# Performance work log

Measured on AMD Instinct MI355X. Metric: run time of the kernel, lower is better.

The kernel has to match this reference:

```python
import jax, jax.numpy as jnp
import numpy as np

ALPHA = 0.2  # LeakyReLU negative slope
NEG_INF = -1e30


def _gat_layer(h, adj_mask, W, a, concat):
    # h: [N, Fin], W: [Fin, Fout], a: [2*Fout]
    Wh = h @ W                      # [N, Fout]
    F = W.shape[1]
    # e_ij = LeakyReLU(a[:F] . Wh_i + a[F:] . Wh_j)  -- equivalent to the
    # concat([Wh_i, Wh_j]) @ a formulation, without the N*N*2F tensor.
    src = Wh @ a[:F]                # [N]
    dst = Wh @ a[F:]                # [N]
    e = src[:, None] + dst[None, :]  # [N, N]
    e = jnp.where(e > 0, e, ALPHA * e)  # LeakyReLU
    e = jnp.where(adj_mask, e, NEG_INF)
    att = jax.nn.softmax(e, axis=1)  # [N, N]; dropout inactive (eval mode)
    h_prime = att @ Wh               # [N, Fout]
    return jax.nn.elu(h_prime) if concat else h_prime


def setup_inputs() -> dict:
    key = jax.random.key(0)
    ks = jax.random.split(key, 6)
    N, nfeat, nhid, nheads, nout = 4096, 512, 256, 4, 256
    x = jax.random.normal(ks[0], (N, nfeat), dtype=jnp.float32)
    adj = jax.random.randint(ks[1], (N, N), 0, 2, dtype=jnp.int32)
    W1 = jax.random.normal(ks[2], (nheads, nfeat, nhid), dtype=jnp.float32) * 0.05
    a1 = jax.random.normal(ks[3], (nheads, 2 * nhid), dtype=jnp.float32) * 0.05
    W2 = jax.random.normal(ks[4], (nhid * nheads, nout), dtype=jnp.float32) * 0.05
    a2 = jax.random.normal(ks[5], (2 * nout,), dtype=jnp.float32) * 0.05
    return {"x": x, "adj": adj, "W1": W1, "a1": a1, "W2": W2, "a2": a2}


def reference(x, adj, W1, a1, W2, a2):
    adj_mask = adj != 0  # [N, N] bool
    # Multi-head first layer (concat=True, ELU), vmapped over heads.
    heads = jax.vmap(lambda W, a: _gat_layer(x, adj_mask, W, a, True))(W1, a1)
    # heads: [nheads, N, nhid] -> concat along features: [N, nheads*nhid]
    h = jnp.transpose(heads, (1, 0, 2)).reshape(x.shape[0], -1)
    # Output attention layer (concat=False).
    return _gat_layer(h, adj_mask, W2, a2, False)
```

## Files before the change

kernel.cpp:

```cpp
#include <hip/hip_runtime.h>
#include <hip/hip_bf16.h>
#include <stdint.h>

#define ALPHA 0.2f
#define LOG2E 1.4426950408889634f

typedef __attribute__((ext_vector_type(4))) float f32x4;
typedef __attribute__((ext_vector_type(8))) __bf16 bf16x8;
typedef __attribute__((ext_vector_type(8))) unsigned short u16x8;
typedef __attribute__((ext_vector_type(4))) unsigned short u16x4;
typedef __attribute__((ext_vector_type(4))) unsigned int u32x4;

static __device__ __forceinline__ unsigned short f2bf(float f) {
  unsigned u = __builtin_bit_cast(unsigned, f);
  u += 0x7FFFu + ((u >> 16) & 1u);
  return (unsigned short)(u >> 16);
}
static __device__ __forceinline__ float bf2f(unsigned short h) {
  unsigned u = ((unsigned)h) << 16;
  return __builtin_bit_cast(float, u);
}
static __device__ __forceinline__ float exp2_hw(float x) {
  float r; asm("v_exp_f32 %0, %1" : "=v"(r) : "v"(x)); return r;
}
static __device__ __forceinline__ unsigned int cvt_pk_bf16(float lo, float hi) {
  unsigned int r; asm("v_cvt_pk_bf16_f32 %0, %1, %2" : "=v"(r) : "v"(lo), "v"(hi)); return r;
}
static __device__ __forceinline__ void gl_lds16(const void* g, void* lds) {
  __builtin_amdgcn_global_load_lds(
      (const __attribute__((address_space(1))) unsigned int*)g,
      (__attribute__((address_space(3))) unsigned int*)lds, 16, 0, 0);
}

#define PREP_PACK_END 65536
#define PREP_CAST_END 66560
#define PREP_T1_END   67072
#define PREP_T2_END   67328
#define PREP_WA1_END  67840
#define PREP_GRID     68096

__global__ void k_prep_all(const int* __restrict__ adj, unsigned int* __restrict__ bits,
                           const float* __restrict__ x, unsigned short* __restrict__ xb,
                           const float* __restrict__ W1, unsigned short* __restrict__ w1t,
                           const float* __restrict__ W2, unsigned short* __restrict__ w2t,
                           const float* __restrict__ a1, float* __restrict__ wa1,
                           const float* __restrict__ a2, float* __restrict__ wa2) {
  __shared__ float tsh[32][33];
  const int b = blockIdx.x, tid = threadIdx.x;
  if (b < PREP_PACK_END) {
    int gid  = b * 4 + (tid >> 6);
    int lane = tid & 63;
    int i   = gid >> 6;
    int w64 = gid & 63;
    int j = (w64 << 6) | lane;
    int v = adj[(long)i * 4096 + j];
    unsigned long long m = __ballot(v != 0);
    if (lane == 0) {
      bits[i * 128 + 2 * w64]     = (unsigned int)m;
      bits[i * 128 + 2 * w64 + 1] = (unsigned int)(m >> 32);
    }
  } else if (b < PREP_CAST_END) {
    int t = (b - PREP_PACK_END) * 256 + tid;
    const f32x4* p = (const f32x4*)(x + (long)t * 8);
    f32x4 va = p[0], vb = p[1];
    u16x8 o;
#pragma unroll
    for (int k = 0; k < 4; ++k) { o[k] = f2bf(va[k]); o[k + 4] = f2bf(vb[k]); }
    *(u16x8*)(xb + (long)t * 8) = o;
  } else if (b < PREP_T2_END) {
    const float* in; unsigned short* out; int K, N, bx, by, bz;
    if (b < PREP_T1_END) {
      int idx = b - PREP_CAST_END;
      bx = idx & 15; by = (idx >> 4) & 7; bz = idx >> 7;
      in = W1; out = w1t; K = 512; N = 256;
    } else {
      int idx = b - PREP_T1_END;
      bx = idx & 31; by = (idx >> 5) & 7; bz = 0;
      in = W2; out = w2t; K = 1024; N = 256;
    }
    long bs = (long)K * N;
    const float* inb = in + bz * bs;
    unsigned short* outb = out + bz * bs;
    int k0 = bx * 32, n0 = by * 32;
    int tx = tid & 31, ty = tid >> 5;
#pragma unroll
    for (int it = 0; it < 4; ++it)
      tsh[ty + it * 8][tx] = inb[(long)(k0 + ty + it * 8) * N + n0 + tx];
    __syncthreads();
#pragma unroll
    for (int it = 0; it < 4; ++it)
      outb[(long)(n0 + ty + it * 8) * K + k0 + tx] = f2bf(tsh[tx][ty + it * 8]);
  } else {
    const float* W; const float* a; float* wa; int headK;
    int bl;
    if (b < PREP_WA1_END) { bl = b - PREP_T2_END; W = W1; a = a1; wa = wa1; headK = 512; }
    else                  { bl = b - PREP_WA1_END; W = W2; a = a2; wa = wa2; headK = 1024; }
    const int F = 256;
    int w = (bl * 256 + tid) >> 6;
    int lane = tid & 63;
    int h = w / headK, fl = w % headK;
    const float* row = W + (size_t)w * F;
    const float* ah = a + (size_t)h * 2 * F;
    float s0 = 0.f, s1 = 0.f;
    for (int fo = lane; fo < F; fo += 64) {
      float wv = row[fo];
      s0 += wv * ah[fo];
      s1 += wv * ah[F + fo];
    }
#pragma unroll
    for (int off = 32; off; off >>= 1) {
      s0 += __shfl_xor(s0, off);
      s1 += __shfl_xor(s1, off);
    }
    if (lane == 0) {
      wa[(size_t)(h * 2 + 0) * headK + fl] = s0;
      wa[(size_t)(h * 2 + 1) * headK + fl] = s1;
    }
  }
}

static __device__ __forceinline__ void gemm_wh_body(
    const unsigned short* __restrict__ A, const unsigned short* __restrict__ BT,
    unsigned short* __restrict__ whT, int K, int i0, int fbase,
    unsigned short* As, unsigned short* Bs) {
  const int tid = threadIdx.x, lane = tid & 63, wid = tid >> 6;
  const int q = lane >> 4, l15 = lane & 15;
  const int wm = wid >> 1, wn = wid & 1;
  f32x4 acc[2][4] = {};
  const unsigned short* aRow = A + (long)(i0 + (tid >> 2)) * K + (tid & 3) * 8;
  for (int kk = 0; kk < K; kk += 32) {
    __syncthreads();
    gl_lds16(aRow + kk, (char*)As + tid * 16);
#pragma unroll
    for (int half = 0; half < 2; ++half) {
      int cid = half * 256 + tid;
      gl_lds16(BT + (long)(fbase + (cid >> 2)) * K + kk + (cid & 3) * 8,
               (char*)Bs + cid * 16);
    }
    __syncthreads();
    bf16x8 af[2], bfr[4];
#pragma unroll
    for (int mi = 0; mi < 2; ++mi)
      af[mi] = *(const bf16x8*)&As[(wm * 32 + mi * 16 + l15) * 32 + q * 8];
#pragma unroll
    for (int ni = 0; ni < 4; ++ni)
      bfr[ni] = *(const bf16x8*)&Bs[(wn * 64 + ni * 16 + l15) * 32 + q * 8];
#pragma unroll
    for (int mi = 0; mi < 2; ++mi)
#pragma unroll
      for (int ni = 0; ni < 4; ++ni)
        acc[mi][ni] = __builtin_amdgcn_mfma_f32_16x16x32_bf16(af[mi], bfr[ni], acc[mi][ni], 0, 0, 0);
  }
#pragma unroll
  for (int mi = 0; mi < 2; ++mi)
#pragma unroll
    for (int ni = 0; ni < 4; ++ni) {
      int ig = i0 + wm * 32 + mi * 16 + q * 4;
      int fg = fbase + wn * 64 + ni * 16 + l15;
      u16x4 v;
#pragma unroll
      for (int r = 0; r < 4; ++r) v[r] = f2bf(acc[mi][ni][r]);
      *(u16x4*)&whT[(long)fg * 4096 + ig] = v;
    }
}

__global__ void __launch_bounds__(256, 4)
k_l1(const unsigned short* __restrict__ xb, const unsigned short* __restrict__ w1t,
     unsigned short* __restrict__ whT1, const float* __restrict__ wa,
     float* __restrict__ srcv, float* __restrict__ dstv, float* __restrict__ dstva) {
  __shared__ unsigned short As[64 * 32];
  __shared__ unsigned short Bs[128 * 32];
  const int b = blockIdx.x;
  if (b < 512) {
    int i0 = (b & 63) * 64;
    int fbase = (b >> 7) * 256 + ((b >> 6) & 1) * 128;
    gemm_wh_body(xb, w1t, whT1, 512, i0, fbase, As, Bs);
    return;
  }
  const int mb = b - 512;
  int lane = threadIdx.x & 63, wid = threadIdx.x >> 6;
  float wv[8][8];
#pragma unroll
  for (int v = 0; v < 8; ++v)
#pragma unroll
    for (int j = 0; j < 8; ++j) wv[v][j] = wa[v * 512 + lane * 8 + j];
  int base = (mb * 4 + wid) * 4;
  for (int rr = 0; rr < 4; ++rr) {
    int i = base + rr;
    u16x8 xv = *(const u16x8*)(xb + (size_t)i * 512 + lane * 8);
    float xf[8];
#pragma unroll
    for (int j = 0; j < 8; ++j) xf[j] = bf2f(xv[j]);
    float s[8] = {};
#pragma unroll
    for (int v = 0; v < 8; ++v)
#pragma unroll
      for (int j = 0; j < 8; ++j) s[v] += xf[j] * wv[v][j];
#pragma unroll
    for (int v = 0; v < 8; ++v)
#pragma unroll
      for (int off = 32; off; off >>= 1) s[v] += __shfl_xor(s[v], off);
    if (lane == 0) {
#pragma unroll
      for (int h = 0; h < 4; ++h) {
        srcv[h * 4096 + i] = s[h * 2] * LOG2E;
        float d = s[h * 2 + 1] * LOG2E;
        dstv[h * 4096 + i] = d;
        dstva[h * 4096 + i] = ALPHA * d;
      }
    }
  }
}

__global__ void __launch_bounds__(256, 4)
k_l2(const unsigned short* __restrict__ h1, const unsigned short* __restrict__ w2t,
     unsigned short* __restrict__ whT2, const float* __restrict__ wa,
     float* __restrict__ srcv, float* __restrict__ dstv, float* __restrict__ dstva) {
  __shared__ unsigned short As[64 * 32];
  __shared__ unsigned short Bs[128 * 32];
  const int b = blockIdx.x;
  if (b < 128) {
    int i0 = (b & 63) * 64;
    int fbase = ((b >> 6) & 1) * 128;
    gemm_wh_body(h1, w2t, whT2, 1024, i0, fbase, As, Bs);
    return;
  }
  const int mb = b - 128;
  int lane = threadIdx.x & 63, wid = threadIdx.x >> 6;
  float wv[2][16];
#pragma unroll
  for (int v = 0; v < 2; ++v)
#pragma unroll
    for (int j = 0; j < 16; ++j) wv[v][j] = wa[v * 1024 + lane * 16 + j];
  int base = (mb * 4 + wid) * 4;
  for (int rr = 0; rr < 4; ++rr) {
    int i = base + rr;
    u16x8 x0 = *(const u16x8*)(h1 + (size_t)i * 1024 + lane * 16);
    u16x8 x1 = *(const u16x8*)(h1 + (size_t)i * 1024 + lane * 16 + 8);
    float s0 = 0.f, s1 = 0.f;
#pragma unroll
    for (int j = 0; j < 8; ++j) {
      float a0 = bf2f(x0[j]), a1 = bf2f(x1[j]);
      s0 += a0 * wv[0][j] + a1 * wv[0][j + 8];
      s1 += a0 * wv[1][j] + a1 * wv[1][j + 8];
    }
#pragma unroll
    for (int off = 32; off; off >>= 1) {
      s0 += __shfl_xor(s0, off);
      s1 += __shfl_xor(s1, off);
    }
    if (lane == 0) {
      srcv[i] = s0 * LOG2E;
      float d = s1 * LOG2E;
      dstv[i] = d;
      dstva[i] = ALPHA * d;
    }
  }
}


#define STAGE(PAR)                                                             \
  _Pragma("unroll")                                                            \
  for (int it = 0; it < 8; ++it)                                               \
    gl_lds16(wh_head + sidx + it * 131072u,                                    \
             (char*)&Bs[PAR][0] + (it * 256 + tid) * 16);                      \
  sidx += 64;

#define PREFETCH(DZ, DA, WB)                                                   \
  _Pragma("unroll")                                                            \
  for (int c4 = 0; c4 < 4; ++c4) {                                             \
    DZ[c4] = *(const f32x4*)(dzp + c4 * 4);                                    \
    DA[c4] = *(const f32x4*)(dap + c4 * 4);                                    \
  }                                                                            \
  WB = *browp;                                                                 \
  dzp += 64; dap += 64; browp += 2;

#define PCOMP(WB, DZ, DA)                                                      \
  {                                                                            \
    unsigned wbv = (WB >> shift) & 0xFFFFu;                                    \
    _Pragma("unroll")                                                          \
    for (int c8 = 0; c8 < 2; ++c8) {                                           \
      float pe[8];                                                             \
      _Pragma("unroll")                                                        \
      for (int jj = 0; jj < 8; ++jj) {                                         \
        float e = fmaxf(sm + DZ[c8 * 2 + (jj >> 2)][jj & 3],                   \
                        am + DA[c8 * 2 + (jj >> 2)][jj & 3]);                  \
        e = (wbv & (1u << (c8 * 8 + jj))) ? e : -1e30f;                        \
        pe[jj] = exp2_hw(e);                                                   \
      }                                                                        \
      u32x4 pv;                                                                \
      pv[0] = cvt_pk_bf16(pe[0], pe[1]);                                       \
      pv[1] = cvt_pk_bf16(pe[2], pe[3]);                                       \
      pv[2] = cvt_pk_bf16(pe[4], pe[5]);                                       \
      pv[3] = cvt_pk_bf16(pe[6], pe[7]);                                       \
      lsum += ((pe[0] + pe[1]) + (pe[2] + pe[3])) +                            \
              ((pe[4] + pe[5]) + (pe[6] + pe[7]));                             \
      if (c8) pvB = pv; else pvA = pv;                                         \
    }                                                                          \
  }

#define PSTO(PAR)                                                              \
  *(u32x4*)&Ps[PAR][prow * 64 + ((2 * kq + 0) ^ (prow & 7)) * 8] = pvA;        \
  *(u32x4*)&Ps[PAR][prow * 64 + ((2 * kq + 1) ^ (prow & 7)) * 8] = pvB;

#define DOMFMA(PAR)                                                            \
  {                                                                            \
    _Pragma("unroll")                                                          \
    for (int s = 0; s < 2; ++s) {                                              \
      bf16x8 af[4], bfr[4];                                                    \
      _Pragma("unroll")                                                        \
      for (int mi = 0; mi < 4; ++mi)                                           \
        af[mi] = *(const bf16x8*)&Ps[PAR][(mi * 16 + l15) * 64 +               \
                                          ((s * 4 + q) ^ (l15 & 7)) * 8];      \
      _Pragma("unroll")                                                        \
      for (int ni = 0; ni < 4; ++ni) {                                         \
        int f = wid * 64 + ni * 16 + l15;                                      \
        int slot = (s * 4 + q) ^ (l15 & 7);                                    \
        bfr[ni] = *(const bf16x8*)&Bs[PAR][f * 64 + slot * 8];                 \
      }                                                                        \
      __builtin_amdgcn_s_setprio(1);                                           \
      _Pragma("unroll")                                                        \
      for (int mi = 0; mi < 4; ++mi)                                           \
        _Pragma("unroll")                                                      \
        for (int ni = 0; ni < 4; ++ni)                                         \
          acc[mi][ni] = __builtin_amdgcn_mfma_f32_16x16x32_bf16(               \
              af[mi], bfr[ni], acc[mi][ni], 0, 0, 0);                          \
      __builtin_amdgcn_s_setprio(0);                                           \
    }                                                                          \
  }

#define STEP_SYNC                                                              \
  asm volatile("s_waitcnt vmcnt(9)" ::: "memory");                             \
  asm volatile("s_waitcnt lgkmcnt(0)" ::: "memory");                           \
  __builtin_amdgcn_sched_barrier(0);                                           \
  __builtin_amdgcn_s_barrier();                                                \
  __builtin_amdgcn_sched_barrier(0);

#define BODY(PAR, DZC, DAC, WBC, DZN, DAN, WBN)                                \
  {                                                                            \
    STAGE(PAR ^ 1)                                                             \
    __builtin_amdgcn_sched_barrier(0);     \
    PREFETCH(DZN, DAN, WBN)                                                    \
    PCOMP(WBC, DZC, DAC)                                                       \
    DOMFMA(PAR)                                                                \
    PSTO(PAR ^ 1)                                                              \
    STEP_SYNC                                                                  \
  }

template <int JS, int H, int OC>
__global__ void __launch_bounds__(256, 2)
k_attn4(const unsigned short* __restrict__ whT, const unsigned int* __restrict__ bits,
        const float* __restrict__ srcv, const float* __restrict__ dstv,
        const float* __restrict__ dstva,
        float* __restrict__ Opart, float* __restrict__ Lpart) {
  static_assert(H * JS == 8, "group size must be 8");
  __shared__ unsigned short Bs[2][256 * 64];
  __shared__ unsigned short Ps[2][64 * 64];
  const int tid = threadIdx.x, lane = tid & 63, wid = tid >> 6;
  const int q = lane >> 4, l15 = lane & 15;
  const int bid = blockIdx.x;
  const int g = bid & 7;
  const int head = g & (H - 1);
  const int js = g / H;
  const int i0 = (bid >> 3) * 64;
  const int jbase = js * (4096 / JS);
  constexpr int JSTEPS = (4096 / JS) / 64;

  const unsigned short* wh_head = whT + (size_t)head * 256 * 4096;
  const int prow = tid & 63, kq = tid >> 6;

  float dmax;
  {
    float* dred = (float*)&Ps[0][0];
    const float* dp = dstv + head * 4096;
    float lm = -1e30f;
#pragma unroll
    for (int k = 0; k < 4; ++k) {
      f32x4 v = *(const f32x4*)(dp + (tid + k * 256) * 4);
      lm = fmaxf(fmaxf(lm, fmaxf(v[0], v[1])), fmaxf(v[2], v[3]));
    }
#pragma unroll
    for (int off = 32; off; off >>= 1) lm = fmaxf(lm, __shfl_xor(lm, off));
    if (lane == 0) dred[wid] = lm;
    __syncthreads();
    dmax = fmaxf(fmaxf(dred[0], dred[1]), fmaxf(dred[2], dred[3]));
    __syncthreads();
  }

  float src_r = srcv[head * 4096 + i0 + prow];
  float m_r;
  { float xm = src_r + dmax; m_r = fmaxf(xm, ALPHA * xm); }
  const float sm = src_r - m_r;
  const float am = ALPHA * src_r - m_r;
  float lsum = 0.f;
  f32x4 acc[4][4] = {};

  const int srow = tid >> 3;
  unsigned sidx = (unsigned)(srow * 4096 + jbase + ((tid & 7) ^ (srow & 7)) * 8);
  const float* dzp = dstv + head * 4096 + jbase + kq * 16;
  const float* dap = dstva + head * 4096 + jbase + kq * 16;
  const unsigned int* browp = bits + (size_t)(i0 + prow) * 128 + (jbase >> 5) + (kq >> 1);
  const int shift = (kq & 1) * 16;

  f32x4 dzA[4], daA[4], dzB[4], daB[4];
  unsigned wbA, wbB;
  u32x4 pvA, pvB;

  PREFETCH(dzA, daA, wbA)
  __builtin_amdgcn_sched_barrier(0);
  STAGE(0)
  __builtin_amdgcn_sched_barrier(0);
  PREFETCH(dzB, daB, wbB)
  PCOMP(wbA, dzA, daA)
  PSTO(0)
  STEP_SYNC

  for (int t = 0; t < JSTEPS - 3; t += 2) {
    BODY(0, dzB, daB, wbB, dzA, daA, wbA)
    BODY(1, dzA, daA, wbA, dzB, daB, wbB)
  }
  BODY(0, dzB, daB, wbB, dzA, daA, wbA)
  DOMFMA(1)

  __syncthreads();
  float* Lred = (float*)&Ps[0][0];
  Lred[kq * 64 + prow] = lsum;
  __syncthreads();
  if (tid < 64)
    Lpart[(size_t)(js * H + head) * 4096 + i0 + tid] =
        Lred[tid] + Lred[64 + tid] + Lred[128 + tid] + Lred[192 + tid];
  float* Ob = Opart + (size_t)js * 4096 * OC + head * 256;
#pragma unroll
  for (int mi = 0; mi < 4; ++mi)
#pragma unroll
    for (int ni = 0; ni < 4; ++ni) {
      int i = i0 + mi * 16 + q * 4;
      int col = wid * 64 + ni * 16 + l15;
#pragma unroll
      for (int r = 0; r < 4; ++r)
        Ob[(size_t)(i + r) * OC + col] = acc[mi][ni][r];
    }
}

__global__ void __launch_bounds__(256) k_comb1(const float* __restrict__ Op,
                                               const float* __restrict__ Lp,
                                               unsigned short* __restrict__ h1) {
  int gidx = blockIdx.x * 256 + threadIdx.x;
  int i = gidx >> 8, c0 = (gidx & 255) * 4;
  int h = c0 >> 8;
  float l = Lp[h * 4096 + i] + Lp[(4 + h) * 4096 + i];
  float inv = 1.f / l;
  f32x4 p0 = *(const f32x4*)(Op + (size_t)i * 1024 + c0);
  f32x4 p1 = *(const f32x4*)(Op + (size_t)4096 * 1024 + (size_t)i * 1024 + c0);
  u16x4 o;
#pragma unroll
  for (int r = 0; r < 4; ++r) {
    float v = (p0[r] + p1[r]) * inv;
    v = v > 0.f ? v : (__expf(v) - 1.f);
    o[r] = f2bf(v);
  }
  *(u16x4*)(h1 + (size_t)i * 1024 + c0) = o;
}

__global__ void __launch_bounds__(256) k_comb2(const float* __restrict__ Op,
                                               const float* __restrict__ Lp,
                                               float* __restrict__ out) {
  int gidx = blockIdx.x * 256 + threadIdx.x;
  int i = gidx >> 6, c0 = (gidx & 63) * 4;
  float l = 0.f;
#pragma unroll
  for (int js = 0; js < 8; ++js) l += Lp[js * 4096 + i];
  f32x4 s = {0.f, 0.f, 0.f, 0.f};
#pragma unroll
  for (int js = 0; js < 8; ++js)
    s += *(const f32x4*)(Op + (size_t)js * 4096 * 256 + (size_t)i * 256 + c0);
  float inv = 1.f / l;
  f32x4 o;
#pragma unroll
  for (int r = 0; r < 4; ++r) o[r] = s[r] * inv;
  *(f32x4*)(out + (size_t)i * 256 + c0) = o;
}

extern "C" void kernel_launch(void* const* d_in, const int* in_sizes, int n_in,
                              void* d_out, int out_size, void* d_ws, size_t ws_size,
                              hipStream_t stream) {
  const float* x  = (const float*)d_in[0];
  const int* adj  = (const int*)d_in[1];
  const float* W1 = (const float*)d_in[2];
  const float* a1 = (const float*)d_in[3];
  const float* W2 = (const float*)d_in[4];
  const float* a2 = (const float*)d_in[5];

  char* ws = (char*)d_ws;
  size_t off = 0;
  auto alloc = [&](size_t bytes) {
    void* p = ws + off;
    off = (off + bytes + 255) & ~(size_t)255;
    return p;
  };
  unsigned int*   bits = (unsigned int*)  alloc((size_t)4096 * 128 * 4);
  unsigned short* xb   = (unsigned short*)alloc((size_t)4096 * 512 * 2);
  unsigned short* w1t  = (unsigned short*)alloc((size_t)4 * 256 * 512 * 2);
  unsigned short* w2t  = (unsigned short*)alloc((size_t)256 * 1024 * 2);
  unsigned short* whT1 = (unsigned short*)alloc((size_t)1024 * 4096 * 2);
  unsigned short* h1   = (unsigned short*)alloc((size_t)4096 * 1024 * 2);
  unsigned short* whT2 = (unsigned short*)alloc((size_t)256 * 4096 * 2);
  float* wa1  = (float*)alloc((size_t)8 * 512 * 4);
  float* wa2  = (float*)alloc((size_t)2 * 1024 * 4);
  float* src1 = (float*)alloc(4 * 4096 * 4);
  float* dst1 = (float*)alloc(4 * 4096 * 4);
  float* dst1a = (float*)alloc(4 * 4096 * 4);
  float* src2 = (float*)alloc(4096 * 4);
  float* dst2 = (float*)alloc(4096 * 4);
  float* dst2a = (float*)alloc(4096 * 4);
  float* Lp1  = (float*)alloc((size_t)8 * 4096 * 4);
  float* Lp2  = (float*)alloc((size_t)8 * 4096 * 4);
  float* Opart = (float*)alloc((size_t)2 * 4096 * 1024 * 4);

  k_prep_all<<<dim3(PREP_GRID), dim3(256), 0, stream>>>(
      adj, bits, x, xb, W1, w1t, W2, w2t, a1, wa1, a2, wa2);

  k_l1<<<dim3(768), dim3(256), 0, stream>>>(xb, w1t, whT1, wa1, src1, dst1, dst1a);
  k_attn4<2, 4, 1024><<<dim3(512), dim3(256), 0, stream>>>(whT1, bits, src1, dst1, dst1a, Opart, Lp1);
  k_comb1<<<dim3(4096), dim3(256), 0, stream>>>(Opart, Lp1, h1);

  k_l2<<<dim3(384), dim3(256), 0, stream>>>(h1, w2t, whT2, wa2, src2, dst2, dst2a);
  k_attn4<8, 1, 256><<<dim3(512), dim3(256), 0, stream>>>(whT2, bits, src2, dst2, dst2a, Opart, Lp2);
  k_comb2<<<dim3(1024), dim3(256), 0, stream>>>(Opart, Lp2, (float*)d_out);
}
```

Before: 246.5 us.

## Double-buffer Wh GEMM LDS staging and move adjacency bit-packing into layer-1 kernel

The Wh GEMM body now double-buffers its global-to-LDS tiles. It prefetches the next K-slice while running MFMAs on the current one, and uses one barrier per iteration instead of two. The adjacency bit-packing moves out of the prep kernel into extra blocks of k_l1, where each block reads int4 vectors and packs nibbles through LDS instead of using per-wave ballots. The goal is to hide load latency in the GEMM and to overlap the bandwidth-heavy adj read with GEMM work. The cost is larger LDS use per block and a bigger k_l1 grid that mixes heterogeneous work.

```diff
diff --git a/kernel.cpp b/kernel.cpp
--- a/kernel.cpp
+++ b/kernel.cpp
@@ -32,35 +32,21 @@
       (__attribute__((address_space(3))) unsigned int*)lds, 16, 0, 0);
 }
 
-#define PREP_PACK_END 65536
-#define PREP_CAST_END 66560
-#define PREP_T1_END   67072
-#define PREP_T2_END   67328
-#define PREP_WA1_END  67840
-#define PREP_GRID     68096
-
-__global__ void k_prep_all(const int* __restrict__ adj, unsigned int* __restrict__ bits,
-                           const float* __restrict__ x, unsigned short* __restrict__ xb,
-                           const float* __restrict__ W1, unsigned short* __restrict__ w1t,
-                           const float* __restrict__ W2, unsigned short* __restrict__ w2t,
-                           const float* __restrict__ a1, float* __restrict__ wa1,
-                           const float* __restrict__ a2, float* __restrict__ wa2) {
+#define PREP_CAST_END 1024
+#define PREP_T1_END   1536
+#define PREP_T2_END   1792
+#define PREP_WA1_END  2304
+#define PREP_GRID     2560
+
+__global__ void k_prep(const float* __restrict__ x, unsigned short* __restrict__ xb,
+                       const float* __restrict__ W1, unsigned short* __restrict__ w1t,
+                       const float* __restrict__ W2, unsigned short* __restrict__ w2t,
+                       const float* __restrict__ a1, float* __restrict__ wa1,
+                       const float* __restrict__ a2, float* __restrict__ wa2) {
   __shared__ float tsh[32][33];
   const int b = blockIdx.x, tid = threadIdx.x;
-  if (b < PREP_PACK_END) {
-    int gid  = b * 4 + (tid >> 6);
-    int lane = tid & 63;
-    int i   = gid >> 6;
-    int w64 = gid & 63;
-    int j = (w64 << 6) | lane;
-    int v = adj[(long)i * 4096 + j];
-    unsigned long long m = __ballot(v != 0);
-    if (lane == 0) {
-      bits[i * 128 + 2 * w64]     = (unsigned int)m;
-      bits[i * 128 + 2 * w64 + 1] = (unsigned int)(m >> 32);
-    }
-  } else if (b < PREP_CAST_END) {
-    int t = (b - PREP_PACK_END) * 256 + tid;
+  if (b < PREP_CAST_END) {
+    int t = b * 256 + tid;
     const f32x4* p = (const f32x4*)(x + (long)t * 8);
     f32x4 va = p[0], vb = p[1];
     u16x8 o;
@@ -121,36 +107,51 @@
 
 static __device__ __forceinline__ void gemm_wh_body(
     const unsigned short* __restrict__ A, const unsigned short* __restrict__ BT,
-    unsigned short* __restrict__ whT, int K, int i0, int fbase,
-    unsigned short* As, unsigned short* Bs) {
+    unsigned short* __restrict__ whT, int K, int i0, int fbase, char* lds) {
+  unsigned short* As = (unsigned short*)lds;
+  unsigned short* Bs = (unsigned short*)(lds + 8192);
   const int tid = threadIdx.x, lane = tid & 63, wid = tid >> 6;
   const int q = lane >> 4, l15 = lane & 15;
   const int wm = wid >> 1, wn = wid & 1;
   f32x4 acc[2][4] = {};
   const unsigned short* aRow = A + (long)(i0 + (tid >> 2)) * K + (tid & 3) * 8;
+  const int cid1 = 256 + tid;
+  const unsigned short* bRow0 = BT + (long)(fbase + (tid >> 2)) * K + (tid & 3) * 8;
+  const unsigned short* bRow1 = BT + (long)(fbase + (cid1 >> 2)) * K + (cid1 & 3) * 8;
+
+#define GSTAGE(PAR, KK)                                                        \
+  gl_lds16(aRow + (KK), lds + (PAR) * 4096 + tid * 16);                        \
+  gl_lds16(bRow0 + (KK), lds + 8192 + (PAR) * 8192 + tid * 16);                \
+  gl_lds16(bRow1 + (KK), lds + 8192 + (PAR) * 8192 + cid1 * 16);
+
+  GSTAGE(0, 0)
+  asm volatile("s_waitcnt vmcnt(0)" ::: "memory");
+  __builtin_amdgcn_sched_barrier(0);
+  __builtin_amdgcn_s_barrier();
   for (int kk = 0; kk < K; kk += 32) {
-    __syncthreads();
-    gl_lds16(aRow + kk, (char*)As + tid * 16);
-#pragma unroll
-    for (int half = 0; half < 2; ++half) {
-      int cid = half * 256 + tid;
-      gl_lds16(BT + (long)(fbase + (cid >> 2)) * K + kk + (cid & 3) * 8,
-               (char*)Bs + cid * 16);
-    }
-    __syncthreads();
+    const int par = (kk >> 5) & 1;
+    if (kk + 32 < K) { GSTAGE(par ^ 1, kk + 32) }
     bf16x8 af[2], bfr[4];
 #pragma unroll
     for (int mi = 0; mi < 2; ++mi)
-      af[mi] = *(const bf16x8*)&As[(wm * 32 + mi * 16 + l15) * 32 + q * 8];
+      af[mi] = *(const bf16x8*)&As[par * 2048 + (wm * 32 + mi * 16 + l15) * 32 + q * 8];
 #pragma unroll
     for (int ni = 0; ni < 4; ++ni)
-      bfr[ni] = *(const bf16x8*)&Bs[(wn * 64 + ni * 16 + l15) * 32 + q * 8];
+      bfr[ni] = *(const bf16x8*)&Bs[par * 4096 + (wn * 64 + ni * 16 + l15) * 32 + q * 8];
+    __builtin_amdgcn_s_setprio(1);
 #pragma unroll
     for (int mi = 0; mi < 2; ++mi)
 #pragma unroll
       for (int ni = 0; ni < 4; ++ni)
         acc[mi][ni] = __builtin_amdgcn_mfma_f32_16x16x32_bf16(af[mi], bfr[ni], acc[mi][ni], 0, 0, 0);
-  }
+    __builtin_amdgcn_s_setprio(0);
+    asm volatile("s_waitcnt vmcnt(0)" ::: "memory");
+    asm volatile("s_waitcnt lgkmcnt(0)" ::: "memory");
+    __builtin_amdgcn_sched_barrier(0);
+    __builtin_amdgcn_s_barrier();
+    __builtin_amdgcn_sched_barrier(0);
+  }
+#undef GSTAGE
 #pragma unroll
   for (int mi = 0; mi < 2; ++mi)
 #pragma unroll
@@ -167,48 +168,66 @@
 __global__ void __launch_bounds__(256, 4)
 k_l1(const unsigned short* __restrict__ xb, const unsigned short* __restrict__ w1t,
      unsigned short* __restrict__ whT1, const float* __restrict__ wa,
-     float* __restrict__ srcv, float* __restrict__ dstv, float* __restrict__ dstva) {
-  __shared__ unsigned short As[64 * 32];
-  __shared__ unsigned short Bs[128 * 32];
-  const int b = blockIdx.x;
+     float* __restrict__ srcv, float* __restrict__ dstv, float* __restrict__ dstva,
+     const int* __restrict__ adj, unsigned int* __restrict__ bits) {
+  __shared__ char lds[24576];
+  const int b = blockIdx.x, tid = threadIdx.x;
   if (b < 512) {
     int i0 = (b & 63) * 64;
     int fbase = (b >> 7) * 256 + ((b >> 6) & 1) * 128;
-    gemm_wh_body(xb, w1t, whT1, 512, i0, fbase, As, Bs);
+    gemm_wh_body(xb, w1t, whT1, 512, i0, fbase, lds);
     return;
   }
-  const int mb = b - 512;
-  int lane = threadIdx.x & 63, wid = threadIdx.x >> 6;
-  float wv[8][8];
-#pragma unroll
-  for (int v = 0; v < 8; ++v)
-#pragma unroll
-    for (int j = 0; j < 8; ++j) wv[v][j] = wa[v * 512 + lane * 8 + j];
-  int base = (mb * 4 + wid) * 4;
-  for (int rr = 0; rr < 4; ++rr) {
-    int i = base + rr;
-    u16x8 xv = *(const u16x8*)(xb + (size_t)i * 512 + lane * 8);
-    float xf[8];
-#pragma unroll
-    for (int j = 0; j < 8; ++j) xf[j] = bf2f(xv[j]);
-    float s[8] = {};
+  if (b < 768) {
+    const int mb = b - 512;
+    int lane = tid & 63, wid = tid >> 6;
+    float wv[8][8];
 #pragma unroll
     for (int v = 0; v < 8; ++v)
 #pragma unroll
-      for (int j = 0; j < 8; ++j) s[v] += xf[j] * wv[v][j];
-#pragma unroll
-    for (int v = 0; v < 8; ++v)
-#pragma unroll
-      for (int off = 32; off; off >>= 1) s[v] += __shfl_xor(s[v], off);
-    if (lane == 0) {
-#pragma unroll
-      for (int h = 0; h < 4; ++h) {
-        srcv[h * 4096 + i] = s[h * 2] * LOG2E;
-        float d = s[h * 2 + 1] * LOG2E;
-        dstv[h * 4096 + i] = d;
-        dstva[h * 4096 + i] = ALPHA * d;
+      for (int j = 0; j < 8; ++j) wv[v][j] = wa[v * 512 + lane * 8 + j];
+    int base = (mb * 4 + wid) * 4;
+    for (int rr = 0; rr < 4; ++rr) {
+      int i = base + rr;
+      u16x8 xv = *(const u16x8*)(xb + (size_t)i * 512 + lane * 8);
+      float xf[8];
+#pragma unroll
+      for (int j = 0; j < 8; ++j) xf[j] = bf2f(xv[j]);
+      float s[8] = {};
+#pragma unroll
+      for (int v = 0; v < 8; ++v)
+#pragma unroll
+        for (int j = 0; j < 8; ++j) s[v] += xf[j] * wv[v][j];
+#pragma unroll
+      for (int v = 0; v < 8; ++v)
+#pragma unroll
+        for (int off = 32; off; off >>= 1) s[v] += __shfl_xor(s[v], off);
+      if (lane == 0) {
+#pragma unroll
+        for (int h = 0; h < 4; ++h) {
+          srcv[h * 4096 + i] = s[h * 2] * LOG2E;
+          float d = s[h * 2 + 1] * LOG2E;
+          dstv[h * 4096 + i] = d;
+          dstva[h * 4096 + i] = ALPHA * d;
+        }
       }
     }
+    return;
+  }
+  int pb = b - 768;
+  int row = pb >> 2, qo = pb & 3;
+  const int4* ap = (const int4*)(adj + (size_t)row * 4096 + qo * 1024);
+  int4 v = ap[tid];
+  unsigned n = (unsigned)(v.x != 0) | ((unsigned)(v.y != 0) << 1) |
+               ((unsigned)(v.z != 0) << 2) | ((unsigned)(v.w != 0) << 3);
+  unsigned char* nib = (unsigned char*)lds;
+  nib[tid] = (unsigned char)n;
+  __syncthreads();
+  if (tid < 32) {
+    unsigned w = 0;
+#pragma unroll
+    for (int s = 0; s < 8; ++s) w |= ((unsigned)nib[tid * 8 + s]) << (4 * s);
+    bits[(size_t)row * 128 + qo * 32 + tid] = w;
   }
 }
 
@@ -216,13 +235,12 @@
 k_l2(const unsigned short* __restrict__ h1, const unsigned short* __restrict__ w2t,
      unsigned short* __restrict__ whT2, const float* __restrict__ wa,
      float* __restrict__ srcv, float* __restrict__ dstv, float* __restrict__ dstva) {
-  __shared__ unsigned short As[64 * 32];
-  __shared__ unsigned short Bs[128 * 32];
+  __shared__ char lds[24576];
   const int b = blockIdx.x;
   if (b < 128) {
     int i0 = (b & 63) * 64;
     int fbase = ((b >> 6) & 1) * 128;
-    gemm_wh_body(h1, w2t, whT2, 1024, i0, fbase, As, Bs);
+    gemm_wh_body(h1, w2t, whT2, 1024, i0, fbase, lds);
     return;
   }
   const int mb = b - 128;
@@ -517,10 +535,10 @@
   float* Lp2  = (float*)alloc((size_t)8 * 4096 * 4);
   float* Opart = (float*)alloc((size_t)2 * 4096 * 1024 * 4);
 
-  k_prep_all<<<dim3(PREP_GRID), dim3(256), 0, stream>>>(
-      adj, bits, x, xb, W1, w1t, W2, w2t, a1, wa1, a2, wa2);
-
-  k_l1<<<dim3(768), dim3(256), 0, stream>>>(xb, w1t, whT1, wa1, src1, dst1, dst1a);
+  k_prep<<<dim3(PREP_GRID), dim3(256), 0, stream>>>(
+      x, xb, W1, w1t, W2, w2t, a1, wa1, a2, wa2);
+
+  k_l1<<<dim3(17152), dim3(256), 0, stream>>>(xb, w1t, whT1, wa1, src1, dst1, dst1a, adj, bits);
   k_attn4<2, 4, 1024><<<dim3(512), dim3(256), 0, stream>>>(whT1, bits, src1, dst1, dst1a, Opart, Lp1);
   k_comb1<<<dim3(4096), dim3(256), 0, stream>>>(Opart, Lp1, h1);
 
```

Result: faster. 230.1 us (-6.7%).
